# Kernel tuning notes

Measured on AMD Instinct MI355X. Metric: run time of the kernel, lower is better.

Reference implementation:

```python
import jax, jax.numpy as jnp
import numpy as np

N, D, H = 100000, 128, 8
C = D // H
E = 800000
NEG_SLOPE = 0.2


def setup_inputs() -> dict:
    key = jax.random.key(0)
    k1, k2, k3, k4, k5, k6 = jax.random.split(key, 6)
    x = jax.random.normal(k1, (N, D), dtype=jnp.float32)
    edge_index = jax.random.randint(k2, (2, E), 0, N, dtype=jnp.int64)
    # GATConv params: shared linear (single node-feature input), per-head attention vectors, bias
    W = jax.random.normal(k3, (D, H * C), dtype=jnp.float32) * (1.0 / np.sqrt(D))
    att_src = jax.random.normal(k4, (H, C), dtype=jnp.float32) * 0.1
    att_dst = jax.random.normal(k5, (H, C), dtype=jnp.float32) * 0.1
    bias = jnp.zeros((H * C,), dtype=jnp.float32)
    return {"x": x, "edge_index": edge_index, "W": W, "att_src": att_src, "att_dst": att_dst, "bias": bias}


def reference(x, edge_index, W, att_src, att_dst, bias):
    # PyG GATConv default: add self-loops
    loops = jnp.tile(jnp.arange(N, dtype=edge_index.dtype), (2, 1))  # [2, N]
    ei = jnp.concatenate([edge_index, loops], axis=1)                # [2, E+N]
    src, dst = ei[0], ei[1]

    h = (x @ W).reshape(N, H, C)                    # [N, H, C]
    a_src = jnp.einsum('nhc,hc->nh', h, att_src)    # [N, H]
    a_dst = jnp.einsum('nhc,hc->nh', h, att_dst)    # [N, H]

    logits = jax.nn.leaky_relu(a_src[src] + a_dst[dst], negative_slope=NEG_SLOPE)  # [Etot, H]

    # segment softmax grouped by destination node (every node has a self-loop -> non-empty)
    mx = jax.ops.segment_max(logits, dst, num_segments=N)   # [N, H]
    ex = jnp.exp(logits - mx[dst])                           # [Etot, H]
    denom = jax.ops.segment_sum(ex, dst, num_segments=N)    # [N, H]
    alpha = ex / (denom[dst] + 1e-16)                        # [Etot, H]

    msg = h[src] * alpha[:, :, None]                         # [Etot, H, C]
    out = jax.ops.segment_sum(msg, dst, num_segments=N)      # [N, H, C]
    out = out.reshape(N, H * C) + bias                       # concat heads
    return out, ei, alpha
```

## Files before the change

### kernel.cpp

```cpp
#include <hip/hip_runtime.h>
#include <hip/hip_bf16.h>
#include <cstdint>

#define N_NODES 100000
#define DIM 128
#define HEADS 8
#define CH 16
#define NEDGE 800000
#define ETOT (NEDGE + N_NODES)
#define NEG_SLOPE 0.2f
#define CAP 32
#define PRE 16

typedef __attribute__((ext_vector_type(8))) short bf16x8;
typedef __attribute__((ext_vector_type(4))) float f32x4;

__device__ __forceinline__ float leaky(float v) {
    return v >= 0.f ? v : NEG_SLOPE * v;
}

__device__ __forceinline__ void wave_lds_fence() {
    asm volatile("s_waitcnt lgkmcnt(0)" ::: "memory");
    __builtin_amdgcn_sched_barrier(0);
}

__device__ __forceinline__ void split2(float w, ushort& hi, ushort& lo) {
    __hip_bfloat16 bh = __float2bfloat16(w);
    float r = w - __bfloat162float(bh);
    __hip_bfloat16 bl = __float2bfloat16(r);
    hi = *(ushort*)&bh;
    lo = *(ushort*)&bl;
}

#define NCOLS 144
#define LDK   136
#define MT    128
#define GEMM_BLOCKS ((N_NODES + MT - 1) / MT)
#define EPB  1536

__global__ __launch_bounds__(512, 4) void fused_kernel(
    const float* __restrict__ x, const float* __restrict__ W,
    const float* __restrict__ att_src, const float* __restrict__ att_dst,
    __hip_bfloat16* __restrict__ h, float* __restrict__ a_src,
    float* __restrict__ a_dst,
    const int* __restrict__ edge_index, float* __restrict__ ei_out,
    int* __restrict__ fill, int2* __restrict__ ebuf2)
{
    __shared__ ushort Whi[NCOLS * LDK];
    __shared__ ushort Wlo[NCOLS * LDK];
    const int tid = threadIdx.x;
    const int bid = blockIdx.x;

    int ee[3], es[3], ed[3];
    #pragma unroll
    for (int t = 0; t < 3; ++t) {
        const int e = bid * EPB + t * 512 + tid;
        ee[t] = e;
        if (e < ETOT) {
            if (e < NEDGE) { es[t] = edge_index[e]; ed[t] = edge_index[NEDGE + e]; }
            else           { es[t] = ed[t] = e - NEDGE; }
        }
    }
    int pos[3];
    #pragma unroll
    for (int t = 0; t < 3; ++t) {
        if (ee[t] < ETOT) {
            ei_out[ee[t]]        = (float)es[t];
            ei_out[ETOT + ee[t]] = (float)ed[t];
            pos[t] = atomicAdd(&fill[ed[t]], 1);
        }
    }

    {
        const int n  = tid >> 2;
        const int kq = (tid & 3) * 32;
        #pragma unroll
        for (int j = 0; j < 32; j += 2) {
            const int k = kq + j;
            float w0 = W[(size_t)k * DIM + n];
            float w1 = W[(size_t)(k + 1) * DIM + n];
            ushort h0, l0, h1, l1;
            split2(w0, h0, l0);
            split2(w1, h1, l1);
            *(uint*)&Whi[n * LDK + k] = (uint)h0 | ((uint)h1 << 16);
            *(uint*)&Wlo[n * LDK + k] = (uint)l0 | ((uint)l1 << 16);
        }
    }
    if (tid < 64) {
        const int t  = tid >> 2;
        const int kq = (tid & 3) * 32;
        const int hd = t & 7;
        const float* av = ((t < 8) ? att_src : att_dst) + hd * CH;
        float avr[CH];
        #pragma unroll
        for (int c = 0; c < CH; ++c) avr[c] = av[c];
        const int nrow = 128 + t;
        for (int j = 0; j < 32; j += 2) {
            const int k = kq + j;
            const float* wp0 = &W[(size_t)k * DIM + hd * CH];
            const float* wp1 = wp0 + DIM;
            float s0 = 0.f, s1 = 0.f;
            #pragma unroll
            for (int c = 0; c < CH; ++c) { s0 += wp0[c] * avr[c]; s1 += wp1[c] * avr[c]; }
            ushort h0, l0, h1, l1;
            split2(s0, h0, l0);
            split2(s1, h1, l1);
            *(uint*)&Whi[nrow * LDK + k] = (uint)h0 | ((uint)h1 << 16);
            *(uint*)&Wlo[nrow * LDK + k] = (uint)l0 | ((uint)l1 << 16);
        }
    }

    #pragma unroll
    for (int t = 0; t < 3; ++t) {
        if (ee[t] < ETOT && pos[t] < CAP)
            ebuf2[ed[t] * CAP + pos[t]] = make_int2(ee[t], es[t]);
    }
    __syncthreads();

    const int w    = tid >> 6;
    const int lane = tid & 63;
    const int r    = lane & 15;
    const int g    = lane >> 4;
    const long arow = (long)bid * MT + w * 16 + r;
    const bool avalid = arow < N_NODES;

    f32x4 acc[9] = {};
    #pragma unroll
    for (int ks = 0; ks < 4; ++ks) {
        const int k0 = ks * 32 + g * 8;
        float xv[8];
        if (avalid) {
            *(float4*)&xv[0] = *(const float4*)&x[arow * DIM + k0];
            *(float4*)&xv[4] = *(const float4*)&x[arow * DIM + k0 + 4];
        } else {
            #pragma unroll
            for (int j = 0; j < 8; ++j) xv[j] = 0.f;
        }
        bf16x8 ahi, alo;
        #pragma unroll
        for (int j = 0; j < 8; ++j) {
            ushort hb, lb;
            split2(xv[j], hb, lb);
            ahi[j] = (short)hb;
            alo[j] = (short)lb;
        }
        #pragma unroll
        for (int nt = 0; nt < 9; ++nt) {
            const int nr = nt * 16 + r;
            bf16x8 bhi = *(const bf16x8*)&Whi[nr * LDK + k0];
            bf16x8 blo = *(const bf16x8*)&Wlo[nr * LDK + k0];
            acc[nt] = __builtin_amdgcn_mfma_f32_16x16x32_bf16(ahi, bhi, acc[nt], 0, 0, 0);
            acc[nt] = __builtin_amdgcn_mfma_f32_16x16x32_bf16(alo, bhi, acc[nt], 0, 0, 0);
            acc[nt] = __builtin_amdgcn_mfma_f32_16x16x32_bf16(ahi, blo, acc[nt], 0, 0, 0);
        }
    }

    const long orow0 = (long)bid * MT + w * 16 + g * 4;
    #pragma unroll
    for (int q = 0; q < 4; ++q) {
        const long orow = orow0 + q;
        if (orow < N_NODES) {
            #pragma unroll
            for (int nt = 0; nt < 8; ++nt)
                h[orow * DIM + nt * 16 + r] = __float2bfloat16(acc[nt][q]);
            const float av = acc[8][q];
            if (r < 8) a_src[orow * HEADS + r]       = av;
            else       a_dst[orow * HEADS + (r - 8)] = av;
        }
    }
}

__global__ __launch_bounds__(256) void gather_kernel(
    const int* __restrict__ fill, const int2* __restrict__ ebuf2,
    const __hip_bfloat16* __restrict__ h,
    const float* __restrict__ a_src, const float* __restrict__ a_dst,
    const float* __restrict__ bias, float* __restrict__ alpha_out,
    float* __restrict__ out)
{
    __shared__ int2  s_es[4][CAP];
    __shared__ float s_al[4][CAP][9];
    const int tid  = threadIdx.x;
    const int w    = tid >> 6;
    const int lane = tid & 63;
    const int n    = blockIdx.x * 4 + w;
    const int head = lane >> 3, c = lane & 7;
    const int chb  = head * CH + c * 2;
    const int dn   = min(fill[n], CAP);
    const float ad = a_dst[(uint)n * HEADS + head];

    if (lane < dn)
        s_es[w][lane] = ebuf2[(uint)n * CAP + lane];
    wave_lds_fence();

    const char* asb = (const char*)a_src;
    const uint  hdo = (uint)(head << 2);
    int   sidx[4];
    float asv[4];
    #pragma unroll
    for (int k = 0; k < 4; ++k) {
        const int i = c + 8 * k;
        if (i < dn) {
            sidx[k] = s_es[w][i].y;
            asv[k]  = *(const float*)(asb + ((uint)sidx[k] * 32u + hdo));
        }
    }

    const char* hb  = (const char*)h;
    const uint  cho = (uint)chb * 2u;
    const int npre = min(dn, PRE);
    unsigned hv[PRE];
    #pragma unroll
    for (int q = 0; q < PRE; ++q) {
        if (q < npre)
            hv[q] = *(const unsigned*)(hb + ((uint)s_es[w][q].y * 256u + cho));
    }

    float lg[4];
    float m = -1e30f;
    #pragma unroll
    for (int k = 0; k < 4; ++k) {
        const int i = c + 8 * k;
        if (i < dn) {
            lg[k] = leaky(asv[k] + ad);
            m = fmaxf(m, lg[k]);
        }
    }
    #pragma unroll
    for (int off = 1; off < 8; off <<= 1)
        m = fmaxf(m, __shfl_xor(m, off));

    float dsum = 0.f;
    #pragma unroll
    for (int k = 0; k < 4; ++k) {
        const int i = c + 8 * k;
        if (i < dn) {
            float ex = __expf(lg[k] - m);
            s_al[w][i][head] = ex;
            dsum += ex;
        }
    }
    #pragma unroll
    for (int off = 1; off < 8; off <<= 1)
        dsum += __shfl_xor(dsum, off);
    const float rdinv = 1.f / (dsum + 1e-16f);
    wave_lds_fence();

    float ax = 0.f, ay = 0.f;
    #pragma unroll
    for (int q = 0; q < PRE; ++q) {
        if (q < npre) {
            float ex = s_al[w][q][head];
            ax += __uint_as_float(hv[q] << 16) * ex;
            ay += __uint_as_float(hv[q] & 0xffff0000u) * ex;
        }
    }
    for (int i = PRE; i < dn; ++i) {
        unsigned hq = *(const unsigned*)(hb + ((uint)s_es[w][i].y * 256u + cho));
        float ex = s_al[w][i][head];
        ax += __uint_as_float(hq << 16) * ex;
        ay += __uint_as_float(hq & 0xffff0000u) * ex;
    }
    ax *= rdinv; ay *= rdinv;
    float2 b = *(const float2*)&bias[chb];
    float2 r; r.x = ax + b.x; r.y = ay + b.y;
    *(float2*)&out[(uint)n * DIM + chb] = r;

    for (int i = c; i < dn; i += 8)
        alpha_out[(uint)s_es[w][i].x * 8u + head] = s_al[w][i][head] * rdinv;
}

extern "C" void kernel_launch(void* const* d_in, const int* in_sizes, int n_in,
                              void* d_out, int out_size, void* d_ws, size_t ws_size,
                              hipStream_t stream) {
    const float* x          = (const float*)d_in[0];
    const int*   edge_index = (const int*)d_in[1];
    const float* W          = (const float*)d_in[2];
    const float* att_src    = (const float*)d_in[3];
    const float* att_dst    = (const float*)d_in[4];
    const float* bias       = (const float*)d_in[5];

    float* out       = (float*)d_out;
    float* ei_out    = out + (size_t)N_NODES * DIM;
    float* alpha_out = ei_out + 2 * (size_t)ETOT;

    __hip_bfloat16* h = (__hip_bfloat16*)d_ws;
    float* a_src = (float*)(h + (size_t)N_NODES * DIM);
    float* a_dst = a_src + (size_t)N_NODES * HEADS;
    int*   fill  = (int*)(a_dst + (size_t)N_NODES * HEADS);
    int2*  ebuf2 = (int2*)(fill + N_NODES);

    hipMemsetAsync(fill, 0, (size_t)N_NODES * sizeof(int), stream);

    fused_kernel<<<GEMM_BLOCKS, 512, 0, stream>>>(
        x, W, att_src, att_dst, h, a_src, a_dst,
        edge_index, ei_out, fill, ebuf2);
    gather_kernel<<<N_NODES / 4, 256, 0, stream>>>(fill, ebuf2, h,
                                                   a_src, a_dst, bias, alpha_out, out);
}
```

Before: 262.8 us.

## Use a fixed 512-block grid so each block amortizes the W split over two GEMM tiles

The fused kernel now launches 512 blocks instead of one per 128-row tile. Each block handles up to two GEMM tiles and 1792 edges, so the per-block cost of loading W, splitting it into hi/lo and writing it to LDS is paid about half as often. The launch-bounds occupancy hint is dropped. In exchange each block does more serial work, and the 782 tiles do not divide evenly over 512 blocks, which leaves a tail imbalance. A small cleanup in the gather kernel drops an unused index array.

```diff
diff --git a/kernel.cpp b/kernel.cpp
--- a/kernel.cpp
+++ b/kernel.cpp
@@ -35,10 +35,11 @@
 #define NCOLS 144
 #define LDK   136
 #define MT    128
-#define GEMM_BLOCKS ((N_NODES + MT - 1) / MT)
-#define EPB  1536
-
-__global__ __launch_bounds__(512, 4) void fused_kernel(
+#define GEMM_TILES ((N_NODES + MT - 1) / MT)
+#define NBLK  512
+#define EPB   1792
+
+__global__ __launch_bounds__(512) void fused_kernel(
     const float* __restrict__ x, const float* __restrict__ W,
     const float* __restrict__ att_src, const float* __restrict__ att_dst,
     __hip_bfloat16* __restrict__ h, float* __restrict__ a_src,
@@ -51,20 +52,23 @@
     const int tid = threadIdx.x;
     const int bid = blockIdx.x;
 
-    int ee[3], es[3], ed[3];
-    #pragma unroll
-    for (int t = 0; t < 3; ++t) {
-        const int e = bid * EPB + t * 512 + tid;
+    int ee[4], es[4], ed[4];
+    bool ev[4];
+    #pragma unroll
+    for (int t = 0; t < 4; ++t) {
+        const int off = t * 512 + tid;
+        const int e = bid * EPB + off;
         ee[t] = e;
-        if (e < ETOT) {
+        ev[t] = (off < EPB) && (e < ETOT);
+        if (ev[t]) {
             if (e < NEDGE) { es[t] = edge_index[e]; ed[t] = edge_index[NEDGE + e]; }
             else           { es[t] = ed[t] = e - NEDGE; }
         }
     }
-    int pos[3];
-    #pragma unroll
-    for (int t = 0; t < 3; ++t) {
-        if (ee[t] < ETOT) {
+    int pos[4];
+    #pragma unroll
+    for (int t = 0; t < 4; ++t) {
+        if (ev[t]) {
             ei_out[ee[t]]        = (float)es[t];
             ei_out[ETOT + ee[t]] = (float)ed[t];
             pos[t] = atomicAdd(&fill[ed[t]], 1);
@@ -111,8 +115,8 @@
     }
 
     #pragma unroll
-    for (int t = 0; t < 3; ++t) {
-        if (ee[t] < ETOT && pos[t] < CAP)
+    for (int t = 0; t < 4; ++t) {
+        if (ev[t] && pos[t] < CAP)
             ebuf2[ed[t] * CAP + pos[t]] = make_int2(ee[t], es[t]);
     }
     __syncthreads();
@@ -121,51 +125,56 @@
     const int lane = tid & 63;
     const int r    = lane & 15;
     const int g    = lane >> 4;
-    const long arow = (long)bid * MT + w * 16 + r;
-    const bool avalid = arow < N_NODES;
-
-    f32x4 acc[9] = {};
-    #pragma unroll
-    for (int ks = 0; ks < 4; ++ks) {
-        const int k0 = ks * 32 + g * 8;
-        float xv[8];
-        if (avalid) {
-            *(float4*)&xv[0] = *(const float4*)&x[arow * DIM + k0];
-            *(float4*)&xv[4] = *(const float4*)&x[arow * DIM + k0 + 4];
-        } else {
+
+    for (int tt = 0; tt < 2; ++tt) {
+        const int tile = bid + tt * NBLK;
+        if (tile >= GEMM_TILES) break;
+        const long arow = (long)tile * MT + w * 16 + r;
+        const bool avalid = arow < N_NODES;
+
+        f32x4 acc[9] = {};
+        #pragma unroll
+        for (int ks = 0; ks < 4; ++ks) {
+            const int k0 = ks * 32 + g * 8;
+            float xv[8];
+            if (avalid) {
+                *(float4*)&xv[0] = *(const float4*)&x[arow * DIM + k0];
+                *(float4*)&xv[4] = *(const float4*)&x[arow * DIM + k0 + 4];
+            } else {
+                #pragma unroll
+                for (int j = 0; j < 8; ++j) xv[j] = 0.f;
+            }
+            bf16x8 ahi, alo;
             #pragma unroll
-            for (int j = 0; j < 8; ++j) xv[j] = 0.f;
-        }
-        bf16x8 ahi, alo;
+            for (int j = 0; j < 8; ++j) {
+                ushort hb, lb;
+                split2(xv[j], hb, lb);
+                ahi[j] = (short)hb;
+                alo[j] = (short)lb;
+            }
+            #pragma unroll
+            for (int nt = 0; nt < 9; ++nt) {
+                const int nr = nt * 16 + r;
+                bf16x8 bhi = *(const bf16x8*)&Whi[nr * LDK + k0];
+                bf16x8 blo = *(const bf16x8*)&Wlo[nr * LDK + k0];
+                acc[nt] = __builtin_amdgcn_mfma_f32_16x16x32_bf16(ahi, bhi, acc[nt], 0, 0, 0);
+                acc[nt] = __builtin_amdgcn_mfma_f32_16x16x32_bf16(alo, bhi, acc[nt], 0, 0, 0);
+                acc[nt] = __builtin_amdgcn_mfma_f32_16x16x32_bf16(ahi, blo, acc[nt], 0, 0, 0);
+            }
+        }
+
+        const long orow0 = (long)tile * MT + w * 16 + g * 4;
         #pragma unroll
-        for (int j = 0; j < 8; ++j) {
-            ushort hb, lb;
-            split2(xv[j], hb, lb);
-            ahi[j] = (short)hb;
-            alo[j] = (short)lb;
-        }
-        #pragma unroll
-        for (int nt = 0; nt < 9; ++nt) {
-            const int nr = nt * 16 + r;
-            bf16x8 bhi = *(const bf16x8*)&Whi[nr * LDK + k0];
-            bf16x8 blo = *(const bf16x8*)&Wlo[nr * LDK + k0];
-            acc[nt] = __builtin_amdgcn_mfma_f32_16x16x32_bf16(ahi, bhi, acc[nt], 0, 0, 0);
-            acc[nt] = __builtin_amdgcn_mfma_f32_16x16x32_bf16(alo, bhi, acc[nt], 0, 0, 0);
-            acc[nt] = __builtin_amdgcn_mfma_f32_16x16x32_bf16(ahi, blo, acc[nt], 0, 0, 0);
-        }
-    }
-
-    const long orow0 = (long)bid * MT + w * 16 + g * 4;
-    #pragma unroll
-    for (int q = 0; q < 4; ++q) {
-        const long orow = orow0 + q;
-        if (orow < N_NODES) {
-            #pragma unroll
-            for (int nt = 0; nt < 8; ++nt)
-                h[orow * DIM + nt * 16 + r] = __float2bfloat16(acc[nt][q]);
-            const float av = acc[8][q];
-            if (r < 8) a_src[orow * HEADS + r]       = av;
-            else       a_dst[orow * HEADS + (r - 8)] = av;
+        for (int q = 0; q < 4; ++q) {
+            const long orow = orow0 + q;
+            if (orow < N_NODES) {
+                #pragma unroll
+                for (int nt = 0; nt < 8; ++nt)
+                    h[orow * DIM + nt * 16 + r] = __float2bfloat16(acc[nt][q]);
+                const float av = acc[8][q];
+                if (r < 8) a_src[orow * HEADS + r]       = av;
+                else       a_dst[orow * HEADS + (r - 8)] = av;
+            }
         }
     }
 }
@@ -194,15 +203,12 @@
 
     const char* asb = (const char*)a_src;
     const uint  hdo = (uint)(head << 2);
-    int   sidx[4];
     float asv[4];
     #pragma unroll
     for (int k = 0; k < 4; ++k) {
         const int i = c + 8 * k;
-        if (i < dn) {
-            sidx[k] = s_es[w][i].y;
-            asv[k]  = *(const float*)(asb + ((uint)sidx[k] * 32u + hdo));
-        }
+        if (i < dn)
+            asv[k] = *(const float*)(asb + ((uint)s_es[w][i].y * 32u + hdo));
     }
 
     const char* hb  = (const char*)h;
@@ -291,7 +297,7 @@
 
     hipMemsetAsync(fill, 0, (size_t)N_NODES * sizeof(int), stream);
 
-    fused_kernel<<<GEMM_BLOCKS, 512, 0, stream>>>(
+    fused_kernel<<<NBLK, 512, 0, stream>>>(
         x, W, att_src, att_dst, h, a_src, a_dst,
         edge_index, ei_out, fill, ebuf2);
     gather_kernel<<<N_NODES / 4, 256, 0, stream>>>(fill, ebuf2, h,
```

New measurement: 271.6 us. 1.03x slower.
